# Performance work log

Measured on AMD Instinct MI355X. Metric: run time of the kernel, lower is better.

The kernel has to match this reference:

```python
import jax, jax.numpy as jnp
import numpy as np

B, S, D, H = 4, 2048, 1024, 16
HD = D // H

def setup_inputs() -> dict:
    key = jax.random.key(0)
    ks = jax.random.split(key, 11)
    s = 1.0 / np.sqrt(D)
    return {
        "q": jax.random.normal(ks[0], (B, S, D), jnp.float32),
        "k": jax.random.normal(ks[1], (B, S, D), jnp.float32),
        "v": jax.random.normal(ks[2], (B, S, D), jnp.float32),
        "Wq": jax.random.normal(ks[3], (D, D), jnp.float32) * s,
        "bq": jax.random.normal(ks[4], (D,), jnp.float32) * 0.01,
        "Wk": jax.random.normal(ks[5], (D, D), jnp.float32) * s,
        "bk": jax.random.normal(ks[6], (D,), jnp.float32) * 0.01,
        "Wv": jax.random.normal(ks[7], (D, D), jnp.float32) * s,
        "bv": jax.random.normal(ks[8], (D,), jnp.float32) * 0.01,
        "Wo": jax.random.normal(ks[9], (D, D), jnp.float32) * s,
        "bo": jax.random.normal(ks[10], (D,), jnp.float32) * 0.01,
    }

def reference(q, k, v, Wq, bq, Wk, bk, Wv, bv, Wo, bo):
    # linear projections + ReLU activation (as in the torch module)
    qh = jax.nn.relu(q @ Wq.T + bq)
    kh = jax.nn.relu(k @ Wk.T + bk)
    vh = jax.nn.relu(v @ Wv.T + bv)
    # split heads: [B,S,D] -> [B,H,S,HD]
    def split(x):
        return x.reshape(B, S, H, HD).transpose(0, 2, 1, 3)
    qh, kh, vh = split(qh), split(kh), split(vh)
    scale = 1.0 / np.sqrt(HD).astype(np.float32)
    scores = jnp.einsum("bhqd,bhkd->bhqk", qh, kh) * scale
    attn = jax.nn.softmax(scores, axis=-1)
    y = jnp.einsum("bhqk,bhkd->bhqd", attn, vh)
    # merge heads: [B,H,S,HD] -> [B,S,D]
    y = y.transpose(0, 2, 1, 3).reshape(B, S, D)
    return jax.nn.relu(y @ Wo.T + bo)
```

## Files before the change

### kernel.cpp

```cpp
#include <hip/hip_runtime.h>
#include <hip/hip_bf16.h>
#include <cstdint>
#include <cstddef>

#define Bc 4
#define Sc 2048
#define Dc 1024
#define Hc 16

typedef __bf16 bf16;
typedef bf16  bf16x4 __attribute__((ext_vector_type(4)));
typedef bf16  bf16x8 __attribute__((ext_vector_type(8)));
typedef float f32x4  __attribute__((ext_vector_type(4)));

__device__ __forceinline__ void load_lds16(const bf16* g, bf16* l) {
    __builtin_amdgcn_global_load_lds((const __attribute__((address_space(1))) void*)g,
                                     (__attribute__((address_space(3))) void*)l,
                                     16, 0, 0);
}

__device__ __forceinline__ void cvt16(const float* __restrict__ g,
                                      bf16x8& lo, bf16x8& hi) {
    const f32x4 a0 = *(const f32x4*)(g);
    const f32x4 a1 = *(const f32x4*)(g + 4);
    const f32x4 a2 = *(const f32x4*)(g + 8);
    const f32x4 a3 = *(const f32x4*)(g + 12);
#pragma unroll
    for (int j = 0; j < 4; j++) {
        lo[j]     = (bf16)a0[j];
        lo[j + 4] = (bf16)a1[j];
        hi[j]     = (bf16)a2[j];
        hi[j + 4] = (bf16)a3[j];
    }
}

__device__ __forceinline__ void store_relu(float* p, float v) { *p = fmaxf(v, 0.0f); }
__device__ __forceinline__ void store_relu(bf16*  p, float v) { *p = (bf16)fmaxf(v, 0.0f); }

__global__ __launch_bounds__(256)
void cvt_f32_bf16(const float* __restrict__ src, bf16* __restrict__ dst, int n16) {
    const int idx = blockIdx.x * 256 + threadIdx.x;
    if (idx >= n16) return;
    bf16x8 lo, hi;
    cvt16(src + (size_t)idx * 16, lo, hi);
    *(bf16x8*)(dst + (size_t)idx * 16)     = lo;
    *(bf16x8*)(dst + (size_t)idx * 16 + 8) = hi;
}

#define BM 128
#define BN 128
#define BK 64

template <typename TC, bool TR>
__global__ __launch_bounds__(256)
void gemm_bb(const bf16* __restrict__ A, const bf16* __restrict__ W,
             const float* __restrict__ bias, TC* __restrict__ C,
             int M, int N, int K) {
    constexpr int POOL = TR ? 36864 : 32768;
    __shared__ __align__(16) char pool[POOL];
    bf16* lA = (bf16*)pool;
    bf16* lB = (bf16*)(pool + 16384);

    const int t    = threadIdx.x;
    const int lane = t & 63;
    const int wave = t >> 6;
    const int l15  = lane & 15;
    const int quad = lane >> 4;

    const int m0 = blockIdx.x * BM;
    const int n0 = blockIdx.y * BN;
    const int wm = (wave >> 1) * 64;
    const int wn = (wave & 1) * 64;

    f32x4 acc[4][4] = {};

    const int srow = t >> 3;
    const int cg   = (((t & 7) ^ (srow & 7)) << 3);
    const bf16* gA = A + (size_t)(m0 + srow) * K + cg;
    const bf16* gW = W + (size_t)(n0 + srow) * K + cg;
    bf16* lA0 = lA + t * 8;
    bf16* lB0 = lB + t * 8;

    for (int k0 = 0; k0 < K; k0 += BK) {
        __syncthreads();
#pragma unroll
        for (int c = 0; c < 4; c++) {
            load_lds16(gA + (size_t)(32 * c) * K, lA0 + c * 2048);
            load_lds16(gW + (size_t)(32 * c) * K, lB0 + c * 2048);
        }
        gA += BK; gW += BK;
        __syncthreads();

#pragma unroll
        for (int ks = 0; ks < 2; ks++) {
            bf16x8 af[4], bfr[4];
#pragma unroll
            for (int mt = 0; mt < 4; mt++) {
                const int row = wm + mt * 16 + l15;
                const int colp = ((((ks << 2) | quad) ^ (l15 & 7)) << 3);
                af[mt] = *(const bf16x8*)(lA + row * BK + colp);
            }
#pragma unroll
            for (int nt = 0; nt < 4; nt++) {
                const int row = wn + nt * 16 + l15;
                const int colp = ((((ks << 2) | quad) ^ (l15 & 7)) << 3);
                bfr[nt] = *(const bf16x8*)(lB + row * BK + colp);
            }
#pragma unroll
            for (int mt = 0; mt < 4; mt++)
#pragma unroll
                for (int nt = 0; nt < 4; nt++)
                    acc[mt][nt] = __builtin_amdgcn_mfma_f32_16x16x32_bf16(
                        af[mt], bfr[nt], acc[mt][nt], 0, 0, 0);
        }
    }

    if constexpr (!TR) {
#pragma unroll
        for (int nt = 0; nt < 4; nt++) {
            const int col = n0 + wn + nt * 16 + l15;
            const float bv = bias[col];
#pragma unroll
            for (int mt = 0; mt < 4; mt++) {
                const int rowb = m0 + wm + mt * 16 + quad * 4;
#pragma unroll
                for (int i = 0; i < 4; i++)
                    store_relu(&C[(size_t)(rowb + i) * N + col], acc[mt][nt][i] + bv);
            }
        }
    } else {
        __syncthreads();
        bf16* trp = (bf16*)pool;
#pragma unroll
        for (int nt = 0; nt < 4; nt++) {
            const int col = n0 + wn + nt * 16 + l15;
            const float bv = bias[col];
#pragma unroll
            for (int mt = 0; mt < 4; mt++)
#pragma unroll
                for (int i = 0; i < 4; i++)
                    trp[((wave * 64) + nt * 16 + l15) * 72 + mt * 16 + quad * 4 + i] =
                        (bf16)fmaxf(acc[mt][nt][i] + bv, 0.0f);
        }
        __syncthreads();
        const int r2 = lane >> 3;
        const int c8 = (lane & 7) * 8;
#pragma unroll
        for (int rr = 0; rr < 8; rr++) {
            const int rt = rr * 8 + r2;
            const bf16x8 vv = *(const bf16x8*)&trp[((wave * 64) + rt) * 72 + c8];
            const int cg2 = n0 + wn + rt;
            const int h   = cg2 >> 6, hd = cg2 & 63;
            const int mg  = m0 + wm + c8;
            const int b   = mg >> 11, s = mg & (Sc - 1);
            bf16* dst = (bf16*)C + ((size_t)(b * Hc + h) * 64 + hd) * Sc + s;
            *(bf16x8*)dst = vv;
        }
    }
}

#define QI 4

__global__ __launch_bounds__(256)
void attn_flash(const bf16* __restrict__ Qh, const bf16* __restrict__ Kh,
                const bf16* __restrict__ Vt_g, bf16* __restrict__ Y) {
    __shared__ __align__(16) bf16 Kl[64][72];
    __shared__ __align__(16) bf16 Vl[64][72];
    __shared__ __align__(16) bf16 Pl[4][64][72];

    const int t    = threadIdx.x;
    const int lane = t & 63;
    const int wave = t >> 6;
    const int l15  = lane & 15;
    const int quad = lane >> 4;

    const int qt = blockIdx.x;
    const int bh = blockIdx.y;
    const int b  = bh >> 4;
    const int h  = bh & 15;
    const int q0 = qt * 256;
    const size_t rowbase = (size_t)b * Sc;
    const size_t vhead   = (size_t)(b * Hc + h) * 64;

    const float qscale = 0.125f * 1.44269504f;
    bf16x8 qf[QI][2];
#pragma unroll
    for (int qi = 0; qi < QI; qi++) {
        const bf16* qp = Qh + (rowbase + q0 + wave * 64 + qi * 16 + l15) * (size_t)Dc + h * 64;
#pragma unroll
        for (int ks = 0; ks < 2; ks++) {
            const bf16x8 raw = *(const bf16x8*)(qp + ks * 32 + quad * 8);
#pragma unroll
            for (int j = 0; j < 8; j++) qf[qi][ks][j] = (bf16)((float)raw[j] * qscale);
        }
    }

    bf16x8 ones;
#pragma unroll
    for (int j = 0; j < 8; j++) ones[j] = (bf16)1.0f;

    f32x4 yacc[QI][4] = {};
    f32x4 sacc[QI]    = {};

    const int sr = t >> 2;
    const int sc = (t & 3) * 16;
    constexpr int NT = Sc / 64;

    const bf16* kp = Kh + (rowbase + sr) * (size_t)Dc + h * 64 + sc;
    const bf16* vp = Vt_g + (vhead + sr) * (size_t)Sc + sc;
    bf16x8 k0 = *(const bf16x8*)kp;
    bf16x8 k1 = *(const bf16x8*)(kp + 8);
    bf16x8 v0 = *(const bf16x8*)vp;
    bf16x8 v1 = *(const bf16x8*)(vp + 8);

    for (int kt = 0; kt < NT; kt++) {
        __syncthreads();
        *(bf16x8*)&Kl[sr][sc]     = k0;
        *(bf16x8*)&Kl[sr][sc + 8] = k1;
        *(bf16x8*)&Vl[sr][sc]     = v0;
        *(bf16x8*)&Vl[sr][sc + 8] = v1;
        __syncthreads();

        if (kt + 1 < NT) {
            kp += (size_t)64 * Dc;
            vp += 64;
            k0 = *(const bf16x8*)kp;
            k1 = *(const bf16x8*)(kp + 8);
            v0 = *(const bf16x8*)vp;
            v1 = *(const bf16x8*)(vp + 8);
        }

        bf16x8 kf[4][2];
#pragma unroll
        for (int mt = 0; mt < 4; mt++) {
            kf[mt][0] = *(const bf16x8*)&Kl[mt * 16 + l15][quad * 8];
            kf[mt][1] = *(const bf16x8*)&Kl[mt * 16 + l15][32 + quad * 8];
        }

#pragma unroll
        for (int qi = 0; qi < QI; qi++) {
            f32x4 s[4];
            __builtin_amdgcn_s_setprio(1);
#pragma unroll
            for (int mt = 0; mt < 4; mt++) {
                s[mt] = (f32x4){0.f, 0.f, 0.f, 0.f};
                s[mt] = __builtin_amdgcn_mfma_f32_16x16x32_bf16(
                    kf[mt][0], qf[qi][0], s[mt], 0, 0, 0);
                s[mt] = __builtin_amdgcn_mfma_f32_16x16x32_bf16(
                    kf[mt][1], qf[qi][1], s[mt], 0, 0, 0);
            }
            __builtin_amdgcn_s_setprio(0);
#pragma unroll
            for (int mt = 0; mt < 4; mt++) {
                bf16x4 pk;
#pragma unroll
                for (int i = 0; i < 4; i++)
                    pk[i] = (bf16)__builtin_amdgcn_exp2f(s[mt][i]);
                *(bf16x4*)&Pl[wave][qi * 16 + l15][mt * 16 + quad * 4] = pk;
            }
        }

        bf16x8 vf[4][2];
#pragma unroll
        for (int nt = 0; nt < 4; nt++) {
            vf[nt][0] = *(const bf16x8*)&Vl[nt * 16 + l15][quad * 8];
            vf[nt][1] = *(const bf16x8*)&Vl[nt * 16 + l15][32 + quad * 8];
        }

        bf16x8 pf[QI][2];
#pragma unroll
        for (int qi = 0; qi < QI; qi++) {
            pf[qi][0] = *(const bf16x8*)&Pl[wave][qi * 16 + l15][quad * 8];
            pf[qi][1] = *(const bf16x8*)&Pl[wave][qi * 16 + l15][32 + quad * 8];
        }
        __builtin_amdgcn_s_setprio(1);
#pragma unroll
        for (int qi = 0; qi < QI; qi++) {
            sacc[qi] = __builtin_amdgcn_mfma_f32_16x16x32_bf16(ones, pf[qi][0], sacc[qi], 0, 0, 0);
            sacc[qi] = __builtin_amdgcn_mfma_f32_16x16x32_bf16(ones, pf[qi][1], sacc[qi], 0, 0, 0);
#pragma unroll
            for (int nt = 0; nt < 4; nt++) {
                yacc[qi][nt] = __builtin_amdgcn_mfma_f32_16x16x32_bf16(
                    vf[nt][0], pf[qi][0], yacc[qi][nt], 0, 0, 0);
                yacc[qi][nt] = __builtin_amdgcn_mfma_f32_16x16x32_bf16(
                    vf[nt][1], pf[qi][1], yacc[qi][nt], 0, 0, 0);
            }
        }
        __builtin_amdgcn_s_setprio(0);
    }

#pragma unroll
    for (int qi = 0; qi < QI; qi++) {
        const float inv = 1.0f / sacc[qi][0];
        bf16* yp = Y + (rowbase + q0 + wave * 64 + qi * 16 + l15) * (size_t)Dc + h * 64;
#pragma unroll
        for (int nt = 0; nt < 4; nt++)
#pragma unroll
            for (int i = 0; i < 4; i++)
                yp[nt * 16 + quad * 4 + i] = (bf16)(yacc[qi][nt][i] * inv);
    }
}

extern "C" void kernel_launch(void* const* d_in, const int* in_sizes, int n_in,
                              void* d_out, int out_size, void* d_ws, size_t ws_size,
                              hipStream_t stream) {
    const float* q  = (const float*)d_in[0];
    const float* k  = (const float*)d_in[1];
    const float* v  = (const float*)d_in[2];
    const float* Wq = (const float*)d_in[3];
    const float* bq = (const float*)d_in[4];
    const float* Wk = (const float*)d_in[5];
    const float* bk = (const float*)d_in[6];
    const float* Wv = (const float*)d_in[7];
    const float* bv = (const float*)d_in[8];
    const float* Wo = (const float*)d_in[9];
    const float* bo = (const float*)d_in[10];
    float* out = (float*)d_out;

    const int M = Bc * Sc;
    const int N = Dc;
    const int K = Dc;
    const size_t E  = (size_t)Bc * Sc * Dc;
    const size_t EW = (size_t)Dc * Dc;

    bf16* Qh   = (bf16*)d_out;
    bf16* Kh   = Qh + E;
    bf16* tmpA = (bf16*)d_ws;
    bf16* VtG  = tmpA + E;
    bf16* Wqb  = VtG + E;
    bf16* Wkb  = Wqb + EW;
    bf16* Wvb  = Wkb + EW;
    bf16* Wob  = Wvb + EW;

    const int n16  = (int)(E / 16);
    const int n16w = (int)(EW / 16);
    dim3 gc(n16 / 256);
    dim3 gw(n16w / 256);
    dim3 gg(M / BM, N / BN);
    dim3 ga(Sc / 256, Bc * Hc);

    cvt_f32_bf16<<<gw, 256, 0, stream>>>(Wq, Wqb, n16w);
    cvt_f32_bf16<<<gw, 256, 0, stream>>>(Wk, Wkb, n16w);
    cvt_f32_bf16<<<gw, 256, 0, stream>>>(Wv, Wvb, n16w);
    cvt_f32_bf16<<<gw, 256, 0, stream>>>(Wo, Wob, n16w);

    cvt_f32_bf16<<<gc, 256, 0, stream>>>(q, tmpA, n16);
    gemm_bb<bf16, false><<<gg, 256, 0, stream>>>(tmpA, Wqb, bq, Qh, M, N, K);

    cvt_f32_bf16<<<gc, 256, 0, stream>>>(k, tmpA, n16);
    gemm_bb<bf16, false><<<gg, 256, 0, stream>>>(tmpA, Wkb, bk, Kh, M, N, K);

    cvt_f32_bf16<<<gc, 256, 0, stream>>>(v, tmpA, n16);
    gemm_bb<bf16, true><<<gg, 256, 0, stream>>>(tmpA, Wvb, bv, VtG, M, N, K);

    attn_flash<<<ga, 256, 0, stream>>>(Qh, Kh, VtG, tmpA);

    gemm_bb<float, false><<<gg, 256, 0, stream>>>(tmpA, Wob, bo, out, M, N, K);
}
```

Measured before the change: 379.7 us.

## Shrink GEMM N-tile, batch weight conversions, swap attention grid order

Halves the GEMM block N-tile from 128 to 64. This doubles the number of blocks, from 512 to 1024 on a 256-CU part, to improve occupancy and wave balance, at the cost of more A-tile reloads and a lower MFMA-to-load ratio. The four weight-conversion launches are merged into one kernel indexed by blockIdx.y, cutting launch overhead. The attention grid is transposed so that consecutive blocks walk batch-head pairs instead of query tiles, which changes L2 locality for K and V.

New measurement: 376.9 us. Within noise of the previous version (-0.7%).

```diff
diff --git a/kernel.cpp b/kernel.cpp
--- a/kernel.cpp
+++ b/kernel.cpp
@@ -47,8 +47,22 @@
     *(bf16x8*)(dst + (size_t)idx * 16 + 8) = hi;
 }
 
+__global__ __launch_bounds__(256)
+void cvt_w4(const float* __restrict__ s0, const float* __restrict__ s1,
+            const float* __restrict__ s2, const float* __restrict__ s3,
+            bf16* __restrict__ dst) {
+    const float* srcs[4] = {s0, s1, s2, s3};
+    const float* src = srcs[blockIdx.y];
+    const int idx = blockIdx.x * 256 + threadIdx.x;
+    bf16x8 lo, hi;
+    cvt16(src + (size_t)idx * 16, lo, hi);
+    bf16* d = dst + (size_t)blockIdx.y * ((size_t)Dc * Dc) + (size_t)idx * 16;
+    *(bf16x8*)d       = lo;
+    *(bf16x8*)(d + 8) = hi;
+}
+
 #define BM 128
-#define BN 128
+#define BN 64
 #define BK 64
 
 template <typename TC, bool TR>
@@ -56,8 +70,7 @@
 void gemm_bb(const bf16* __restrict__ A, const bf16* __restrict__ W,
              const float* __restrict__ bias, TC* __restrict__ C,
              int M, int N, int K) {
-    constexpr int POOL = TR ? 36864 : 32768;
-    __shared__ __align__(16) char pool[POOL];
+    __shared__ __align__(16) char pool[24576];
     bf16* lA = (bf16*)pool;
     bf16* lB = (bf16*)(pool + 16384);
 
@@ -70,9 +83,9 @@
     const int m0 = blockIdx.x * BM;
     const int n0 = blockIdx.y * BN;
     const int wm = (wave >> 1) * 64;
-    const int wn = (wave & 1) * 64;
-
-    f32x4 acc[4][4] = {};
+    const int wn = (wave & 1) * 32;
+
+    f32x4 acc[4][2] = {};
 
     const int srow = t >> 3;
     const int cg   = (((t & 7) ^ (srow & 7)) << 3);
@@ -84,32 +97,32 @@
     for (int k0 = 0; k0 < K; k0 += BK) {
         __syncthreads();
 #pragma unroll
-        for (int c = 0; c < 4; c++) {
+        for (int c = 0; c < 4; c++)
             load_lds16(gA + (size_t)(32 * c) * K, lA0 + c * 2048);
+#pragma unroll
+        for (int c = 0; c < 2; c++)
             load_lds16(gW + (size_t)(32 * c) * K, lB0 + c * 2048);
-        }
         gA += BK; gW += BK;
         __syncthreads();
 
 #pragma unroll
         for (int ks = 0; ks < 2; ks++) {
-            bf16x8 af[4], bfr[4];
+            bf16x8 af[4], bfr[2];
+            const int colp = ((((ks << 2) | quad) ^ (l15 & 7)) << 3);
 #pragma unroll
             for (int mt = 0; mt < 4; mt++) {
                 const int row = wm + mt * 16 + l15;
-                const int colp = ((((ks << 2) | quad) ^ (l15 & 7)) << 3);
                 af[mt] = *(const bf16x8*)(lA + row * BK + colp);
             }
 #pragma unroll
-            for (int nt = 0; nt < 4; nt++) {
+            for (int nt = 0; nt < 2; nt++) {
                 const int row = wn + nt * 16 + l15;
-                const int colp = ((((ks << 2) | quad) ^ (l15 & 7)) << 3);
                 bfr[nt] = *(const bf16x8*)(lB + row * BK + colp);
             }
 #pragma unroll
             for (int mt = 0; mt < 4; mt++)
 #pragma unroll
-                for (int nt = 0; nt < 4; nt++)
+                for (int nt = 0; nt < 2; nt++)
                     acc[mt][nt] = __builtin_amdgcn_mfma_f32_16x16x32_bf16(
                         af[mt], bfr[nt], acc[mt][nt], 0, 0, 0);
         }
@@ -117,7 +130,7 @@
 
     if constexpr (!TR) {
 #pragma unroll
-        for (int nt = 0; nt < 4; nt++) {
+        for (int nt = 0; nt < 2; nt++) {
             const int col = n0 + wn + nt * 16 + l15;
             const float bv = bias[col];
 #pragma unroll
@@ -132,23 +145,23 @@
         __syncthreads();
         bf16* trp = (bf16*)pool;
 #pragma unroll
-        for (int nt = 0; nt < 4; nt++) {
+        for (int nt = 0; nt < 2; nt++) {
             const int col = n0 + wn + nt * 16 + l15;
             const float bv = bias[col];
 #pragma unroll
             for (int mt = 0; mt < 4; mt++)
 #pragma unroll
                 for (int i = 0; i < 4; i++)
-                    trp[((wave * 64) + nt * 16 + l15) * 72 + mt * 16 + quad * 4 + i] =
+                    trp[((wave * 32) + nt * 16 + l15) * 72 + mt * 16 + quad * 4 + i] =
                         (bf16)fmaxf(acc[mt][nt][i] + bv, 0.0f);
         }
         __syncthreads();
         const int r2 = lane >> 3;
         const int c8 = (lane & 7) * 8;
 #pragma unroll
-        for (int rr = 0; rr < 8; rr++) {
+        for (int rr = 0; rr < 4; rr++) {
             const int rt = rr * 8 + r2;
-            const bf16x8 vv = *(const bf16x8*)&trp[((wave * 64) + rt) * 72 + c8];
+            const bf16x8 vv = *(const bf16x8*)&trp[((wave * 32) + rt) * 72 + c8];
             const int cg2 = n0 + wn + rt;
             const int h   = cg2 >> 6, hd = cg2 & 63;
             const int mg  = m0 + wm + c8;
@@ -174,8 +187,8 @@
     const int l15  = lane & 15;
     const int quad = lane >> 4;
 
-    const int qt = blockIdx.x;
-    const int bh = blockIdx.y;
+    const int bh = blockIdx.x;
+    const int qt = blockIdx.y;
     const int b  = bh >> 4;
     const int h  = bh & 15;
     const int q0 = qt * 256;
@@ -335,14 +348,11 @@
     const int n16  = (int)(E / 16);
     const int n16w = (int)(EW / 16);
     dim3 gc(n16 / 256);
-    dim3 gw(n16w / 256);
+    dim3 gw4(n16w / 256, 4);
     dim3 gg(M / BM, N / BN);
-    dim3 ga(Sc / 256, Bc * Hc);
-
-    cvt_f32_bf16<<<gw, 256, 0, stream>>>(Wq, Wqb, n16w);
-    cvt_f32_bf16<<<gw, 256, 0, stream>>>(Wk, Wkb, n16w);
-    cvt_f32_bf16<<<gw, 256, 0, stream>>>(Wv, Wvb, n16w);
-    cvt_f32_bf16<<<gw, 256, 0, stream>>>(Wo, Wob, n16w);
+    dim3 ga(Bc * Hc, Sc / 256);
+
+    cvt_w4<<<gw4, 256, 0, stream>>>(Wq, Wk, Wv, Wo, Wqb);
 
     cvt_f32_bf16<<<gc, 256, 0, stream>>>(q, tmpA, n16);
     gemm_bb<bf16, false><<<gg, 256, 0, stream>>>(tmpA, Wqb, bq, Qh, M, N, K);
```
